# Kernel optimization log

Measured on AMD Instinct MI355X. Metric: run time of the kernel, lower is better.

The kernel has to match this reference:

```python
import jax, jax.numpy as jnp
import numpy as np

B, C, D, H, CS = 2, 1024, 512, 8, 64  # batch, bindings, d_binding, heads, chunk_size


def setup_inputs() -> dict:
    key = jax.random.key(0)
    ks = jax.random.split(key, 12)
    d = D // H
    def lin(k, out_f, in_f):
        return jax.random.normal(k, (out_f, in_f), jnp.float32) * (1.0 / np.sqrt(in_f))
    return {
        "x": jax.random.normal(ks[0], (B, C, D), jnp.float32),
        "Wq": lin(ks[1], D, D), "bq": jnp.zeros((D,), jnp.float32),
        "Wk": lin(ks[2], D, D), "bk": jnp.zeros((D,), jnp.float32),
        "Wv": lin(ks[3], D, D), "bv": jnp.zeros((D,), jnp.float32),
        "w1": lin(ks[4], d, 3 * d), "b1": jnp.zeros((d,), jnp.float32),
        "w2": lin(ks[5], 1, d), "b2": jnp.zeros((1,), jnp.float32),
        "Wo": lin(ks[6], D, D), "bo": jnp.zeros((D,), jnp.float32),
    }


def reference(x, Wq, bq, Wk, bk, Wv, bv, w1, b1, w2, b2, Wo, bo):
    Bx, Cx, Dx = x.shape
    d = Dx // H
    def heads(W, b):
        y = jnp.einsum('bcD,eD->bce', x, W) + b
        return y.reshape(Bx, Cx, H, d).transpose(0, 2, 1, 3)  # (B,H,C,d)
    q = heads(Wq, bq)
    k = heads(Wk, bk)
    v = heads(Wv, bv)
    # split first MLP layer weight into q / k / q*k blocks
    w1_q, w1_k, w1_qk = w1[:, :d], w1[:, d:2 * d], w1[:, 2 * d:]
    qp = jnp.einsum('bhcd,ed->bhce', q, w1_q)  # (B,H,C,d)
    kp = jnp.einsum('bhcd,ed->bhce', k, w1_k)  # (B,H,C,d)
    nc = Cx // CS
    q_ch = q.reshape(Bx, H, nc, CS, d).transpose(2, 0, 1, 3, 4)   # (nc,B,H,CS,d)
    qp_ch = qp.reshape(Bx, H, nc, CS, d).transpose(2, 0, 1, 3, 4)
    inv_sqrt_d = jnp.float32(1.0 / np.sqrt(d))

    def step(carry, xs):
        qc, qpc = xs  # (B,H,CS,d) each
        # hidden: (B,H,CS,C,d)
        res = qpc[:, :, :, None, :] + kp[:, :, None, :, :] + b1
        inter = qc[:, :, :, None, :] * k[:, :, None, :, :]
        hid = res + jnp.einsum('bhijd,ed->bhije', inter, w1_qk)
        h = jax.nn.gelu(hid, approximate=False)
        scores = (jnp.einsum('bhije,e->bhij', h, w2[0]) + b2[0]) * inv_sqrt_d
        attn = jax.nn.softmax(scores, axis=-1)  # (B,H,CS,C)
        out = jnp.einsum('bhij,bhjd->bhid', attn, v)  # (B,H,CS,d)
        return carry, out

    _, outs = jax.lax.scan(jax.checkpoint(step), None, (q_ch, qp_ch))  # (nc,B,H,CS,d)
    out = outs.transpose(1, 2, 0, 3, 4).reshape(Bx, H, Cx, d)
    out = out.transpose(0, 2, 1, 3).reshape(Bx, Cx, Dx)
    return jnp.einsum('bcD,eD->bce', out, Wo) + bo
```

## Files before the change

### kernel.cpp

```cpp
#include <hip/hip_runtime.h>
#include <cstdint>

typedef unsigned short u16;
typedef unsigned int u32;
typedef __attribute__((ext_vector_type(8))) short short8;
typedef __attribute__((ext_vector_type(4))) float floatx4;

__device__ __forceinline__ float b2f(u16 u) {
    union { unsigned int i; float f; } c; c.i = ((unsigned int)u) << 16; return c.f;
}
__device__ __forceinline__ u16 f2b(float f) {
    union { float f; unsigned int i; } c; c.f = f;
    unsigned int u = c.i;
    u = u + 0x7FFFu + ((u >> 16) & 1u);
    return (u16)(u >> 16);
}
__device__ __forceinline__ float u2f(u32 u) { union { u32 u; float f; } c; c.u = u; return c.f; }

__global__ __launch_bounds__(256) void gemm_qkv(
    const float* __restrict__ x,
    const float* __restrict__ Wq, const float* __restrict__ Wk, const float* __restrict__ Wv,
    const float* __restrict__ bq, const float* __restrict__ bk, const float* __restrict__ bv,
    float* __restrict__ qout, u16* __restrict__ kout,
    u16* __restrict__ vthi, u16* __restrict__ vtlo)
{
    __shared__ u16 xs[64 * 72];
    __shared__ u16 wsl[64 * 72];
    int tid = threadIdx.x;
    int lane = tid & 63;
    int wv = tid >> 6;
    int lo = lane & 15, hi = lane >> 4;
    int which = blockIdx.y >> 3;
    int m0 = blockIdx.x * 64, n0 = (blockIdx.y & 7) * 64;
    const float* W    = which == 0 ? Wq : (which == 1 ? Wk : Wv);
    const float* bias = which == 0 ? bq : (which == 1 ? bk : bv);

    floatx4 acc[4];
#pragma unroll
    for (int mt = 0; mt < 4; ++mt) acc[mt] = (floatx4){0.f, 0.f, 0.f, 0.f};

    for (int k0 = 0; k0 < 512; k0 += 64) {
        __syncthreads();
#pragma unroll
        for (int i = 0; i < 2; ++i) {
            int v = tid + i * 256;
            int row = v >> 3, c8 = (v & 7) * 8;
            const float* ap = x + (m0 + row) * 512 + k0 + c8;
            const float* wp = W + (n0 + row) * 512 + k0 + c8;
            float4 a0 = *(const float4*)(ap);
            float4 a1 = *(const float4*)(ap + 4);
            float4 w0 = *(const float4*)(wp);
            float4 w1v = *(const float4*)(wp + 4);
            union { u16 u[8]; uint4 q; } ca, cw;
            ca.u[0] = f2b(a0.x); ca.u[1] = f2b(a0.y); ca.u[2] = f2b(a0.z); ca.u[3] = f2b(a0.w);
            ca.u[4] = f2b(a1.x); ca.u[5] = f2b(a1.y); ca.u[6] = f2b(a1.z); ca.u[7] = f2b(a1.w);
            cw.u[0] = f2b(w0.x); cw.u[1] = f2b(w0.y); cw.u[2] = f2b(w0.z); cw.u[3] = f2b(w0.w);
            cw.u[4] = f2b(w1v.x); cw.u[5] = f2b(w1v.y); cw.u[6] = f2b(w1v.z); cw.u[7] = f2b(w1v.w);
            *(uint4*)(xs + row * 72 + c8)  = ca.q;
            *(uint4*)(wsl + row * 72 + c8) = cw.q;
        }
        __syncthreads();
#pragma unroll
        for (int ks = 0; ks < 2; ++ks) {
            short8 bfr = *(const short8*)(wsl + (wv * 16 + lo) * 72 + ks * 32 + hi * 8);
#pragma unroll
            for (int mt = 0; mt < 4; ++mt) {
                short8 afr = *(const short8*)(xs + (mt * 16 + lo) * 72 + ks * 32 + hi * 8);
                acc[mt] = __builtin_amdgcn_mfma_f32_16x16x32_bf16(afr, bfr, acc[mt], 0, 0, 0);
            }
        }
    }

    int n = n0 + wv * 16 + lo;
    float bv2 = bias[n];
    if (which == 2) {
        __syncthreads();
        int nl = wv * 16 + lo;
#pragma unroll
        for (int mt = 0; mt < 4; ++mt)
#pragma unroll
            for (int r = 0; r < 4; ++r) {
                int ml = mt * 16 + hi * 4 + r;
                float y = acc[mt][r] + bv2;
                u16 vh = f2b(y);
                u16 vl = f2b(y - b2f(vh));
                xs[nl * 72 + ml]  = vh;
                wsl[nl * 72 + ml] = vl;
            }
        __syncthreads();
        int row = tid >> 2, seg = (tid & 3) * 16;
        int b = m0 >> 10, c0 = m0 & 1023, h2 = n0 >> 6;
        size_t dst = ((size_t)((b * 8 + h2) * 64 + row)) * 1024 + c0 + seg;
        *(uint4*)(vthi + dst)     = *(uint4*)(xs  + row * 72 + seg);
        *(uint4*)(vthi + dst + 8) = *(uint4*)(xs  + row * 72 + seg + 8);
        *(uint4*)(vtlo + dst)     = *(uint4*)(wsl + row * 72 + seg);
        *(uint4*)(vtlo + dst + 8) = *(uint4*)(wsl + row * 72 + seg + 8);
    } else {
        int h = n >> 6, dd = n & 63;
#pragma unroll
        for (int mt = 0; mt < 4; ++mt)
#pragma unroll
            for (int r = 0; r < 4; ++r) {
                int m = m0 + mt * 16 + hi * 4 + r;
                float y = acc[mt][r] + bv2;
                int b = m >> 10, c = m & 1023;
                int idx = (((b * 8 + h) * 1024) + c) * 64 + dd;
                if (which == 0) qout[idx] = y;
                else            kout[idx] = f2b(y);
            }
    }
}

__global__ __launch_bounds__(256) void gemm_out(
    const float* __restrict__ A, const float* __restrict__ W, const float* __restrict__ bias,
    float* __restrict__ outf)
{
    __shared__ u16 xs[64 * 72];
    __shared__ u16 wsl[64 * 72];
    int tid = threadIdx.x;
    int lane = tid & 63;
    int wv = tid >> 6;
    int lo = lane & 15, hi = lane >> 4;
    int m0 = blockIdx.x * 64, n0 = blockIdx.y * 64;

    floatx4 acc[4];
#pragma unroll
    for (int mt = 0; mt < 4; ++mt) acc[mt] = (floatx4){0.f, 0.f, 0.f, 0.f};

    for (int k0 = 0; k0 < 512; k0 += 64) {
        __syncthreads();
#pragma unroll
        for (int i = 0; i < 2; ++i) {
            int v = tid + i * 256;
            int row = v >> 3, c8 = (v & 7) * 8;
            const float* ap = A + (m0 + row) * 512 + k0 + c8;
            const float* wp = W + (n0 + row) * 512 + k0 + c8;
            float4 a0 = *(const float4*)(ap);
            float4 a1 = *(const float4*)(ap + 4);
            float4 w0 = *(const float4*)(wp);
            float4 w1v = *(const float4*)(wp + 4);
            union { u16 u[8]; uint4 q; } ca, cw;
            ca.u[0] = f2b(a0.x); ca.u[1] = f2b(a0.y); ca.u[2] = f2b(a0.z); ca.u[3] = f2b(a0.w);
            ca.u[4] = f2b(a1.x); ca.u[5] = f2b(a1.y); ca.u[6] = f2b(a1.z); ca.u[7] = f2b(a1.w);
            cw.u[0] = f2b(w0.x); cw.u[1] = f2b(w0.y); cw.u[2] = f2b(w0.z); cw.u[3] = f2b(w0.w);
            cw.u[4] = f2b(w1v.x); cw.u[5] = f2b(w1v.y); cw.u[6] = f2b(w1v.z); cw.u[7] = f2b(w1v.w);
            *(uint4*)(xs + row * 72 + c8)  = ca.q;
            *(uint4*)(wsl + row * 72 + c8) = cw.q;
        }
        __syncthreads();
#pragma unroll
        for (int ks = 0; ks < 2; ++ks) {
            short8 bfr = *(const short8*)(wsl + (wv * 16 + lo) * 72 + ks * 32 + hi * 8);
#pragma unroll
            for (int mt = 0; mt < 4; ++mt) {
                short8 afr = *(const short8*)(xs + (mt * 16 + lo) * 72 + ks * 32 + hi * 8);
                acc[mt] = __builtin_amdgcn_mfma_f32_16x16x32_bf16(afr, bfr, acc[mt], 0, 0, 0);
            }
        }
    }

    int n = n0 + wv * 16 + lo;
    float bv = bias[n];
#pragma unroll
    for (int mt = 0; mt < 4; ++mt)
#pragma unroll
        for (int r = 0; r < 4; ++r) {
            int m = m0 + mt * 16 + hi * 4 + r;
            outf[m * 512 + n] = acc[mt][r] + bv;
        }
}

__global__ __launch_bounds__(256, 4) void attn14(
    const float* __restrict__ qf, const u16* __restrict__ kb,
    const u16* __restrict__ vthi, const u16* __restrict__ vtlo,
    const float* __restrict__ w1, const float* __restrict__ b1, const float* __restrict__ w2,
    float* __restrict__ ao)
{
    __shared__ float q_l[4 * 64];
    __shared__ __align__(16) u16 plds[2][512];
    __shared__ float l_sh[4];
    int tid = threadIdx.x;
    int lane = tid & 63;
    int wv = tid >> 6;
    int lo = lane & 15, hi = lane >> 4;
    int bh = blockIdx.x >> 8;
    int qbase = (blockIdx.x & 255) << 2;
    int qi = qbase | wv;

    const float NA = -2.45546696f;

    if (tid < 128) { uint4 z; z.x = z.y = z.z = z.w = 0u; ((uint4*)plds)[tid] = z; }

    q_l[wv * 64 + lane] = qf[(bh * 1024 + qi) * 64 + lane];

    float qpacc = b1[lane];
#pragma unroll
    for (int d8 = 0; d8 < 64; d8 += 8) {
        float4 wa = *(const float4*)(w1 + lane * 192 + d8);
        float4 wb = *(const float4*)(w1 + lane * 192 + d8 + 4);
        const float* q8 = q_l + wv * 64 + d8;
        qpacc = __builtin_fmaf(q8[0], wa.x, qpacc);
        qpacc = __builtin_fmaf(q8[1], wa.y, qpacc);
        qpacc = __builtin_fmaf(q8[2], wa.z, qpacc);
        qpacc = __builtin_fmaf(q8[3], wa.w, qpacc);
        qpacc = __builtin_fmaf(q8[4], wb.x, qpacc);
        qpacc = __builtin_fmaf(q8[5], wb.y, qpacc);
        qpacc = __builtin_fmaf(q8[6], wb.z, qpacc);
        qpacc = __builtin_fmaf(q8[7], wb.w, qpacc);
    }
    qpacc *= NA;

    u32 wcp[4][2];
    float w2row = w2[lane] * -0.07344288f;
#pragma unroll
    for (int mt = 0; mt < 4; ++mt)
#pragma unroll
        for (int h2 = 0; h2 < 2; ++h2) {
            int e0 = mt * 16 + hi * 4 + h2 * 2;
            u32 lo16 = (u32)f2b(__shfl(w2row, e0));
            u32 hi16 = (u32)f2b(__shfl(w2row, e0 + 1));
            wcp[mt][h2] = (hi16 << 16) | lo16;
        }

    float qv2[2][8];
#pragma unroll
    for (int ks = 0; ks < 2; ++ks)
#pragma unroll
        for (int j = 0; j < 8; ++j)
            qv2[ks][j] = q_l[wv * 64 + ks * 32 + hi * 8 + j];

    short8 af[4][2];
#pragma unroll
    for (int mt = 0; mt < 4; ++mt) {
        const float* wr = w1 + (mt * 16 + lo) * 192;
#pragma unroll
        for (int ks = 0; ks < 2; ++ks) {
            int dd0 = ks * 32 + hi * 8;
            float4 a0 = *(const float4*)(wr + 128 + dd0);
            float4 a1 = *(const float4*)(wr + 128 + dd0 + 4);
            float4 k0 = *(const float4*)(wr + 64 + dd0);
            float4 k1 = *(const float4*)(wr + 64 + dd0 + 4);
            union { u16 u[8]; short8 s; } cv;
            cv.u[0] = f2b(NA * __builtin_fmaf(qv2[ks][0], a0.x, k0.x));
            cv.u[1] = f2b(NA * __builtin_fmaf(qv2[ks][1], a0.y, k0.y));
            cv.u[2] = f2b(NA * __builtin_fmaf(qv2[ks][2], a0.z, k0.z));
            cv.u[3] = f2b(NA * __builtin_fmaf(qv2[ks][3], a0.w, k0.w));
            cv.u[4] = f2b(NA * __builtin_fmaf(qv2[ks][4], a1.x, k1.x));
            cv.u[5] = f2b(NA * __builtin_fmaf(qv2[ks][5], a1.y, k1.y));
            cv.u[6] = f2b(NA * __builtin_fmaf(qv2[ks][6], a1.z, k1.z));
            cv.u[7] = f2b(NA * __builtin_fmaf(qv2[ks][7], a1.w, k1.w));
            af[mt][ks] = cv.s;
        }
    }

    floatx4 qpinit[4];
    {
        const floatx4 z = (floatx4){0.f, 0.f, 0.f, 0.f};
        union { u16 u[8]; short8 s; } bb;
#pragma unroll
        for (int i = 0; i < 8; ++i) bb.u[i] = 0;
        bb.u[0] = (hi == 0) ? (u16)0x3F80 : (u16)0;
#pragma unroll
        for (int mt = 0; mt < 4; ++mt) {
            float qpv = __shfl(qpacc, mt * 16 + lo);
            union { u16 u[8]; short8 s; } aa;
#pragma unroll
            for (int i = 0; i < 8; ++i) aa.u[i] = 0;
            aa.u[0] = (hi == 0) ? f2b(qpv) : (u16)0;
            qpinit[mt] = __builtin_amdgcn_mfma_f32_16x16x32_bf16(aa.s, bb.s, z, 0, 0, 0);
        }
    }

    float l_run = 0.f;
    floatx4 pvacc = (floatx4){0.f, 0.f, 0.f, 0.f};
    const u16* kbase = kb + bh * 65536;
    const u16* vhb = vthi + bh * 65536 + (wv * 16 + lo) * 1024 + hi * 8;
    const u16* vlb = vtlo + bh * 65536 + (wv * 16 + lo) * 1024 + hi * 8;

    short8 bf[2][2];
#pragma unroll
    for (int t = 0; t < 2; ++t)
#pragma unroll
        for (int ks = 0; ks < 2; ++ks) {
            uint4 kv = *(const uint4*)(kbase + (t * 16 + lo) * 64 + ks * 32 + hi * 8);
            bf[t][ks] = *(short8*)&kv;
        }

    for (int j0 = 0; j0 < 1024; j0 += 32) {
        uint4 vhq = *(const uint4*)(vhb + j0);
        uint4 vlq = *(const uint4*)(vlb + j0);

        float s0a = 0.f, s0b = 0.f, s1a = 0.f, s1b = 0.f;

        floatx4 aP[2], aN[2];
        aP[0] = __builtin_amdgcn_mfma_f32_16x16x32_bf16(af[0][0], bf[0][0], qpinit[0], 0, 0, 0);
        aP[0] = __builtin_amdgcn_mfma_f32_16x16x32_bf16(af[0][1], bf[0][1], aP[0], 0, 0, 0);
        aP[1] = __builtin_amdgcn_mfma_f32_16x16x32_bf16(af[0][0], bf[1][0], qpinit[0], 0, 0, 0);
        aP[1] = __builtin_amdgcn_mfma_f32_16x16x32_bf16(af[0][1], bf[1][1], aP[1], 0, 0, 0);

#pragma unroll
        for (int mt = 0; mt < 4; ++mt) {
            if (mt < 3) {
                aN[0] = __builtin_amdgcn_mfma_f32_16x16x32_bf16(af[mt + 1][0], bf[0][0], qpinit[mt + 1], 0, 0, 0);
                aN[0] = __builtin_amdgcn_mfma_f32_16x16x32_bf16(af[mt + 1][1], bf[0][1], aN[0], 0, 0, 0);
                aN[1] = __builtin_amdgcn_mfma_f32_16x16x32_bf16(af[mt + 1][0], bf[1][0], qpinit[mt + 1], 0, 0, 0);
                aN[1] = __builtin_amdgcn_mfma_f32_16x16x32_bf16(af[mt + 1][1], bf[1][1], aN[1], 0, 0, 0);
            } else {
                int jn = (j0 + 32) & 1023;
#pragma unroll
                for (int t = 0; t < 2; ++t)
#pragma unroll
                    for (int ks = 0; ks < 2; ++ks) {
                        uint4 kv = *(const uint4*)(kbase + (jn + t * 16 + lo) * 64 + ks * 32 + hi * 8);
                        bf[t][ks] = *(short8*)&kv;
                    }
            }

#pragma unroll
            for (int h2 = 0; h2 < 2; ++h2) {
                u32 wp = wcp[mt][h2];
                float w0 = u2f(wp << 16);
                float w1v = u2f(wp & 0xFFFF0000u);
#pragma unroll
                for (int t = 0; t < 2; ++t) {
                    float x0 = aP[t][h2 * 2 + 0];
                    float x1 = aP[t][h2 * 2 + 1];
                    float a0 = 1.0f + __builtin_amdgcn_exp2f(x0);
                    float a1 = 1.0f + __builtin_amdgcn_exp2f(x1);
                    float rc = __builtin_amdgcn_rcpf(a0 * a1);
                    if (t == 0) {
                        s0a = __builtin_fmaf(x0 * w0,  rc * a1, s0a);
                        s0b = __builtin_fmaf(x1 * w1v, rc * a0, s0b);
                    } else {
                        s1a = __builtin_fmaf(x0 * w0,  rc * a1, s1a);
                        s1b = __builtin_fmaf(x1 * w1v, rc * a0, s1b);
                    }
                }
            }
            aP[0] = aN[0];
            aP[1] = aN[1];
        }

        float s0 = s0a + s0b, s1 = s1a + s1b;
        s0 += __shfl_xor(s0, 16); s0 += __shfl_xor(s0, 32);
        s1 += __shfl_xor(s1, 16); s1 += __shfl_xor(s1, 32);

        float p0 = __builtin_amdgcn_exp2f(s0 - 16.0f);
        float p1 = __builtin_amdgcn_exp2f(s1 - 16.0f);
        u16 ph0 = f2b(p0);
        u16 ph1 = f2b(p1);
        l_run += b2f(ph0) + b2f(ph1);

        u16* pw = (u16*)plds[(j0 >> 5) & 1];
        if (lane < 16) {
            pw[((lo >> 3) * 16 + wv) * 8 + (lo & 7)] = ph0;
            pw[((2 + (lo >> 3)) * 16 + wv) * 8 + (lo & 7)] = ph1;
        }
        __syncthreads();

        short8 pf = *(const short8*)(pw + lane * 8);
        pvacc = __builtin_amdgcn_mfma_f32_16x16x32_bf16(pf, *(short8*)&vhq, pvacc, 0, 0, 0);
        pvacc = __builtin_amdgcn_mfma_f32_16x16x32_bf16(pf, *(short8*)&vlq, pvacc, 0, 0, 0);
    }

    float l = l_run;
    l += __shfl_xor(l, 1); l += __shfl_xor(l, 2);
    l += __shfl_xor(l, 4); l += __shfl_xor(l, 8);
    if (lane == 0) l_sh[wv] = l;
    __syncthreads();

    if (hi == 0) {
        int b = bh >> 3, h = bh & 7;
#pragma unroll
        for (int q = 0; q < 4; ++q) {
            float outv = pvacc[q] * __builtin_amdgcn_rcpf(l_sh[q]);
            ao[((b * 1024 + qbase + q) * 512) + h * 64 + wv * 16 + lo] = outv;
        }
    }
}

extern "C" void kernel_launch(void* const* d_in, const int* in_sizes, int n_in,
                              void* d_out, int out_size, void* d_ws, size_t ws_size,
                              hipStream_t stream)
{
    (void)in_sizes; (void)n_in; (void)out_size; (void)ws_size;
    const float* x  = (const float*)d_in[0];
    const float* Wq = (const float*)d_in[1];
    const float* bq = (const float*)d_in[2];
    const float* Wk = (const float*)d_in[3];
    const float* bk = (const float*)d_in[4];
    const float* Wv = (const float*)d_in[5];
    const float* bv = (const float*)d_in[6];
    const float* w1 = (const float*)d_in[7];
    const float* b1 = (const float*)d_in[8];
    const float* w2 = (const float*)d_in[9];
    const float* Wo = (const float*)d_in[11];
    const float* bo = (const float*)d_in[12];

    char* ws = (char*)d_ws;
    float* q_ws = (float*)(ws);
    u16*   k_ws = (u16*)(ws + (4u << 20));
    u16*   vthi = (u16*)(ws + (6u << 20));
    u16*   vtlo = (u16*)(ws + (8u << 20));
    float* a_ws = (float*)(ws + (10u << 20));

    dim3 blk(256);
    hipLaunchKernelGGL(gemm_qkv, dim3(32, 24), blk, 0, stream,
                       x, Wq, Wk, Wv, bq, bk, bv, q_ws, k_ws, vthi, vtlo);
    hipLaunchKernelGGL(attn14, dim3(4096), blk, 0, stream,
                       q_ws, k_ws, vthi, vtlo, w1, b1, w2, a_ws);
    hipLaunchKernelGGL(gemm_out, dim3(32, 8), blk, 0, stream, a_ws, Wo, bo, (float*)d_out);
}
```

Measured before the change: 555.6 us.

## Batch four key chunks per barrier and stagger key start per block

The attention loop now computes scores for four 32-key chunks before a single LDS write and __syncthreads, and then runs four PV MFMA pairs. Previously there was one barrier per 32 keys, so this cuts barriers by a factor of four. Each block also starts at a rotated key offset (joff), which spreads concurrent blocks across different K/V rows and should reduce cache and channel contention. The cost is a larger padded LDS buffer, more live registers for the packed probabilities, and V loads that are no longer issued ahead of the score compute.

```diff
diff --git a/kernel.cpp b/kernel.cpp
--- a/kernel.cpp
+++ b/kernel.cpp
@@ -170,14 +170,14 @@
         }
 }
 
-__global__ __launch_bounds__(256, 4) void attn14(
+__global__ __launch_bounds__(256, 4) void attn16(
     const float* __restrict__ qf, const u16* __restrict__ kb,
     const u16* __restrict__ vthi, const u16* __restrict__ vtlo,
     const float* __restrict__ w1, const float* __restrict__ b1, const float* __restrict__ w2,
     float* __restrict__ ao)
 {
     __shared__ float q_l[4 * 64];
-    __shared__ __align__(16) u16 plds[2][512];
+    __shared__ __align__(16) u16 plds[2 * 4 * 528];
     __shared__ float l_sh[4];
     int tid = threadIdx.x;
     int lane = tid & 63;
@@ -186,10 +186,11 @@
     int bh = blockIdx.x >> 8;
     int qbase = (blockIdx.x & 255) << 2;
     int qi = qbase | wv;
+    int joff = ((blockIdx.x & 31) << 5);
 
     const float NA = -2.45546696f;
 
-    if (tid < 128) { uint4 z; z.x = z.y = z.z = z.w = 0u; ((uint4*)plds)[tid] = z; }
+    for (int i = tid; i < (2 * 4 * 528) / 2; i += 256) ((u32*)plds)[i] = 0;
 
     q_l[wv * 64 + lane] = qf[(bh * 1024 + qi) * 64 + lane];
 
@@ -271,6 +272,8 @@
         }
     }
 
+    __syncthreads();
+
     float l_run = 0.f;
     floatx4 pvacc = (floatx4){0.f, 0.f, 0.f, 0.f};
     const u16* kbase = kb + bh * 65536;
@@ -282,85 +285,97 @@
     for (int t = 0; t < 2; ++t)
 #pragma unroll
         for (int ks = 0; ks < 2; ++ks) {
-            uint4 kv = *(const uint4*)(kbase + (t * 16 + lo) * 64 + ks * 32 + hi * 8);
+            uint4 kv = *(const uint4*)(kbase + (joff + t * 16 + lo) * 64 + ks * 32 + hi * 8);
             bf[t][ks] = *(short8*)&kv;
         }
 
-    for (int j0 = 0; j0 < 1024; j0 += 32) {
-        uint4 vhq = *(const uint4*)(vhb + j0);
-        uint4 vlq = *(const uint4*)(vlb + j0);
-
-        float s0a = 0.f, s0b = 0.f, s1a = 0.f, s1b = 0.f;
-
-        floatx4 aP[2], aN[2];
-        aP[0] = __builtin_amdgcn_mfma_f32_16x16x32_bf16(af[0][0], bf[0][0], qpinit[0], 0, 0, 0);
-        aP[0] = __builtin_amdgcn_mfma_f32_16x16x32_bf16(af[0][1], bf[0][1], aP[0], 0, 0, 0);
-        aP[1] = __builtin_amdgcn_mfma_f32_16x16x32_bf16(af[0][0], bf[1][0], qpinit[0], 0, 0, 0);
-        aP[1] = __builtin_amdgcn_mfma_f32_16x16x32_bf16(af[0][1], bf[1][1], aP[1], 0, 0, 0);
-
-#pragma unroll
-        for (int mt = 0; mt < 4; ++mt) {
-            if (mt < 3) {
-                aN[0] = __builtin_amdgcn_mfma_f32_16x16x32_bf16(af[mt + 1][0], bf[0][0], qpinit[mt + 1], 0, 0, 0);
-                aN[0] = __builtin_amdgcn_mfma_f32_16x16x32_bf16(af[mt + 1][1], bf[0][1], aN[0], 0, 0, 0);
-                aN[1] = __builtin_amdgcn_mfma_f32_16x16x32_bf16(af[mt + 1][0], bf[1][0], qpinit[mt + 1], 0, 0, 0);
-                aN[1] = __builtin_amdgcn_mfma_f32_16x16x32_bf16(af[mt + 1][1], bf[1][1], aN[1], 0, 0, 0);
-            } else {
-                int jn = (j0 + 32) & 1023;
-#pragma unroll
-                for (int t = 0; t < 2; ++t)
-#pragma unroll
-                    for (int ks = 0; ks < 2; ++ks) {
-                        uint4 kv = *(const uint4*)(kbase + (jn + t * 16 + lo) * 64 + ks * 32 + hi * 8);
-                        bf[t][ks] = *(short8*)&kv;
-                    }
-            }
-
-#pragma unroll
-            for (int h2 = 0; h2 < 2; ++h2) {
-                u32 wp = wcp[mt][h2];
-                float w0 = u2f(wp << 16);
-                float w1v = u2f(wp & 0xFFFF0000u);
-#pragma unroll
-                for (int t = 0; t < 2; ++t) {
-                    float x0 = aP[t][h2 * 2 + 0];
-                    float x1 = aP[t][h2 * 2 + 1];
-                    float a0 = 1.0f + __builtin_amdgcn_exp2f(x0);
-                    float a1 = 1.0f + __builtin_amdgcn_exp2f(x1);
-                    float rc = __builtin_amdgcn_rcpf(a0 * a1);
-                    if (t == 0) {
-                        s0a = __builtin_fmaf(x0 * w0,  rc * a1, s0a);
-                        s0b = __builtin_fmaf(x1 * w1v, rc * a0, s0b);
-                    } else {
-                        s1a = __builtin_fmaf(x0 * w0,  rc * a1, s1a);
-                        s1b = __builtin_fmaf(x1 * w1v, rc * a0, s1b);
+    for (int g = 0; g < 8; ++g) {
+        u32 st0 = 0, st1 = 0, st2 = 0, st3 = 0;
+#pragma unroll
+        for (int c = 0; c < 4; ++c) {
+            int jc = (g * 128 + c * 32 + joff) & 1023;
+            int jn = (jc + 32) & 1023;
+
+            float s0a = 0.f, s0b = 0.f, s1a = 0.f, s1b = 0.f;
+
+            floatx4 aP[2], aN[2];
+            aP[0] = __builtin_amdgcn_mfma_f32_16x16x32_bf16(af[0][0], bf[0][0], qpinit[0], 0, 0, 0);
+            aP[0] = __builtin_amdgcn_mfma_f32_16x16x32_bf16(af[0][1], bf[0][1], aP[0], 0, 0, 0);
+            aP[1] = __builtin_amdgcn_mfma_f32_16x16x32_bf16(af[0][0], bf[1][0], qpinit[0], 0, 0, 0);
+            aP[1] = __builtin_amdgcn_mfma_f32_16x16x32_bf16(af[0][1], bf[1][1], aP[1], 0, 0, 0);
+
+#pragma unroll
+            for (int mt = 0; mt < 4; ++mt) {
+                if (mt < 3) {
+                    aN[0] = __builtin_amdgcn_mfma_f32_16x16x32_bf16(af[mt + 1][0], bf[0][0], qpinit[mt + 1], 0, 0, 0);
+                    aN[0] = __builtin_amdgcn_mfma_f32_16x16x32_bf16(af[mt + 1][1], bf[0][1], aN[0], 0, 0, 0);
+                    aN[1] = __builtin_amdgcn_mfma_f32_16x16x32_bf16(af[mt + 1][0], bf[1][0], qpinit[mt + 1], 0, 0, 0);
+                    aN[1] = __builtin_amdgcn_mfma_f32_16x16x32_bf16(af[mt + 1][1], bf[1][1], aN[1], 0, 0, 0);
+                } else {
+#pragma unroll
+                    for (int t = 0; t < 2; ++t)
+#pragma unroll
+                        for (int ks = 0; ks < 2; ++ks) {
+                            uint4 kv = *(const uint4*)(kbase + (jn + t * 16 + lo) * 64 + ks * 32 + hi * 8);
+                            bf[t][ks] = *(short8*)&kv;
+                        }
+                }
+
+#pragma unroll
+                for (int h2 = 0; h2 < 2; ++h2) {
+                    u32 wp = wcp[mt][h2];
+                    float w0 = u2f(wp << 16);
+                    float w1v = u2f(wp & 0xFFFF0000u);
+#pragma unroll
+                    for (int t = 0; t < 2; ++t) {
+                        float x0 = aP[t][h2 * 2 + 0];
+                        float x1 = aP[t][h2 * 2 + 1];
+                        float a0 = 1.0f + __builtin_amdgcn_exp2f(x0);
+                        float a1 = 1.0f + __builtin_amdgcn_exp2f(x1);
+                        float rc = __builtin_amdgcn_rcpf(a0 * a1);
+                        if (t == 0) {
+                            s0a = __builtin_fmaf(x0 * w0,  rc * a1, s0a);
+                            s0b = __builtin_fmaf(x1 * w1v, rc * a0, s0b);
+                        } else {
+                            s1a = __builtin_fmaf(x0 * w0,  rc * a1, s1a);
+                            s1b = __builtin_fmaf(x1 * w1v, rc * a0, s1b);
+                        }
                     }
                 }
+                aP[0] = aN[0];
+                aP[1] = aN[1];
             }
-            aP[0] = aN[0];
-            aP[1] = aN[1];
-        }
-
-        float s0 = s0a + s0b, s1 = s1a + s1b;
-        s0 += __shfl_xor(s0, 16); s0 += __shfl_xor(s0, 32);
-        s1 += __shfl_xor(s1, 16); s1 += __shfl_xor(s1, 32);
-
-        float p0 = __builtin_amdgcn_exp2f(s0 - 16.0f);
-        float p1 = __builtin_amdgcn_exp2f(s1 - 16.0f);
-        u16 ph0 = f2b(p0);
-        u16 ph1 = f2b(p1);
-        l_run += b2f(ph0) + b2f(ph1);
-
-        u16* pw = (u16*)plds[(j0 >> 5) & 1];
-        if (lane < 16) {
-            pw[((lo >> 3) * 16 + wv) * 8 + (lo & 7)] = ph0;
-            pw[((2 + (lo >> 3)) * 16 + wv) * 8 + (lo & 7)] = ph1;
-        }
-        __syncthreads();
-
-        short8 pf = *(const short8*)(pw + lane * 8);
-        pvacc = __builtin_amdgcn_mfma_f32_16x16x32_bf16(pf, *(short8*)&vhq, pvacc, 0, 0, 0);
-        pvacc = __builtin_amdgcn_mfma_f32_16x16x32_bf16(pf, *(short8*)&vlq, pvacc, 0, 0, 0);
+
+            float s0 = s0a + s0b, s1 = s1a + s1b;
+            s0 += __shfl_xor(s0, 16); s0 += __shfl_xor(s0, 32);
+            s1 += __shfl_xor(s1, 16); s1 += __shfl_xor(s1, 32);
+
+            float p0 = __builtin_amdgcn_exp2f(s0 - 16.0f);
+            float p1 = __builtin_amdgcn_exp2f(s1 - 16.0f);
+            u16 ph0 = f2b(p0);
+            u16 ph1 = f2b(p1);
+            u32 pk = ((u32)ph1 << 16) | (u32)ph0;
+            l_run += b2f(ph0) + b2f(ph1);
+            if (c == 0) st0 = pk; else if (c == 1) st1 = pk;
+            else if (c == 2) st2 = pk; else st3 = pk;
+        }
+
+        u16* pw = plds + (g & 1) * (4 * 528);
+        u32 sv = (hi == 0) ? st0 : (hi == 1) ? st1 : (hi == 2) ? st2 : st3;
+        int wb = hi * 528 + wv * 8 + (lo & 7);
+        pw[wb + (lo >> 3) * 128]       = (u16)sv;
+        pw[wb + (2 + (lo >> 3)) * 128] = (u16)(sv >> 16);
+        __syncthreads();
+
+#pragma unroll
+        for (int c = 0; c < 4; ++c) {
+            int jg = (g * 128 + c * 32 + joff) & 1023;
+            uint4 vh = *(const uint4*)(vhb + jg);
+            uint4 vl = *(const uint4*)(vlb + jg);
+            short8 pf = *(const short8*)(pw + c * 528 + lane * 8);
+            pvacc = __builtin_amdgcn_mfma_f32_16x16x32_bf16(pf, *(short8*)&vh, pvacc, 0, 0, 0);
+            pvacc = __builtin_amdgcn_mfma_f32_16x16x32_bf16(pf, *(short8*)&vl, pvacc, 0, 0, 0);
+        }
     }
 
     float l = l_run;
@@ -407,7 +422,7 @@
     dim3 blk(256);
     hipLaunchKernelGGL(gemm_qkv, dim3(32, 24), blk, 0, stream,
                        x, Wq, Wk, Wv, bq, bk, bv, q_ws, k_ws, vthi, vtlo);
-    hipLaunchKernelGGL(attn14, dim3(4096), blk, 0, stream,
+    hipLaunchKernelGGL(attn16, dim3(4096), blk, 0, stream,
                        q_ws, k_ws, vthi, vtlo, w1, b1, w2, a_ws);
     hipLaunchKernelGGL(gemm_out, dim3(32, 8), blk, 0, stream, a_ws, Wo, bo, (float*)d_out);
 }
```

New measurement: 1.179 ms. +112.1%, slower.
